# Optimization experiments

Measured on AMD Instinct MI355X. Metric: run time of the kernel, lower is better.

## Reference

```python
import jax, jax.numpy as jnp
from jax import lax
import numpy as np

UNITS = 128
IN_DIM = 512
BATCH = 128
SEQ = 1024


def setup_inputs() -> dict:
    key = jax.random.key(0)
    k1, k2, k3 = jax.random.split(key, 3)
    x = jax.random.normal(k1, (BATCH, SEQ, IN_DIM), dtype=jnp.float32)
    # glorot-ish scaling for stability
    W = jax.random.normal(k2, (IN_DIM, 4 * UNITS), dtype=jnp.float32) * (1.0 / np.sqrt(IN_DIM))
    U = jax.random.normal(k3, (UNITS, 4 * UNITS), dtype=jnp.float32) * (1.0 / np.sqrt(UNITS))
    b = jnp.zeros((4 * UNITS,), dtype=jnp.float32)
    return {"x": x, "W": W, "U": U, "b": b}


def reference(x, W, U, b):
    # Keras LSTM with activation='tanh' AND recurrent_activation='tanh'
    # (all four gates use tanh, unlike the standard sigmoid gates).
    # Gate order in Keras kernels: i, f, g(cell candidate), o.
    B = x.shape[0]
    units = U.shape[0]
    # Precompute input projections for all timesteps: [T, B, 4*units]
    xW = jnp.einsum('bti,ij->tbj', x, W) + b

    def step(carry, xw_t):
        h, c = carry
        z = xw_t + h @ U  # [B, 4*units]
        i, f, g, o = jnp.split(z, 4, axis=-1)
        i = jnp.tanh(i)
        f = jnp.tanh(f)
        g = jnp.tanh(g)
        o = jnp.tanh(o)
        c_new = f * c + i * g
        h_new = o * jnp.tanh(c_new)
        return (h_new, c_new), None

    h0 = jnp.zeros((B, units), dtype=x.dtype)
    c0 = jnp.zeros((B, units), dtype=x.dtype)
    (h_last, _), _ = lax.scan(step, (h0, c0), xW)
    return h_last  # [B, units] (return_sequences=False)
```

## Files before the change

kernel.cpp:

```cpp
#include <hip/hip_runtime.h>
#include <hip/hip_bf16.h>


#define UNITS 128
#define IN_DIM 512
#define BATCH 128
#define SEQ 1024
#define GATES 512
#define M_ROWS (BATCH * SEQ)

typedef __attribute__((ext_vector_type(8))) short short8;
typedef __attribute__((ext_vector_type(4))) float floatx4;
typedef __attribute__((ext_vector_type(4))) float fv4;
typedef __attribute__((ext_vector_type(2))) float fv2;

__device__ __forceinline__ unsigned short f2bf(float f) {
    unsigned int x = __builtin_bit_cast(unsigned int, f);
    unsigned int r = (x + 0x7fffu + ((x >> 16) & 1u)) >> 16;
    return (unsigned short)r;
}
__device__ __forceinline__ float bf2f(unsigned short u) {
    unsigned int x = ((unsigned int)u) << 16;
    return __builtin_bit_cast(float, x);
}
__device__ __forceinline__ unsigned int pack2(float lo, float hi) {
    return (unsigned int)f2bf(lo) | ((unsigned int)f2bf(hi) << 16);
}

__device__ __forceinline__ float fast_tanh(float x) {
    float y = fminf(34.6f, fmaxf(-34.6f, x * 2.88539008f));
    float e = __builtin_amdgcn_exp2f(y);
    return 1.0f - 2.0f * __builtin_amdgcn_rcpf(e + 1.0f);
}

template <int CTRL>
__device__ __forceinline__ float dppf(float x) {
    int xi = __builtin_bit_cast(int, x);
    int r = __builtin_amdgcn_update_dpp(0, xi, CTRL, 0xF, 0xF, true);
    return __builtin_bit_cast(float, r);
}
#define DPP_XOR1 0xB1
#define DPP_XOR2 0x4E
#define DPP_BC0 0x00
#define DPP_BC1 0x55
#define DPP_BC2 0xAA
#define DPP_BC3 0xFF

__device__ __forceinline__ void pk_fma(fv2& acc, fv2 a, fv2 b) {
    asm("v_pk_fma_f32 %0, %1, %2, %0" : "+v"(acc) : "v"(a), "v"(b));
}

__global__ void k_wt(const float* __restrict__ W, unsigned short* __restrict__ Wt) {
    int idx = blockIdx.x * 256 + threadIdx.x;
    int n = idx >> 9;
    int k = idx & 511;
    Wt[idx] = f2bf(W[k * 512 + n]);
}

template <bool XWF32>
__global__ void __launch_bounds__(256, 2)
k_gemm(const float* __restrict__ A, const unsigned short* __restrict__ Bt,
       void* __restrict__ Cout) {
    __shared__ __align__(16) unsigned short As[128 * 40];
    __shared__ __align__(16) unsigned short Bs[128 * 40];
    const int tid = threadIdx.x;
    const int m0 = blockIdx.y << 7;
    const int n0 = blockIdx.x << 7;
    const int l = tid & 63;
    const int w = tid >> 6;
    const int wr = (w >> 1) << 6;
    const int wc = (w & 1) << 6;
    const int lrow = l & 15;
    const int lq = l >> 4;

    floatx4 acc[4][4] = {};

    const int srow = tid >> 1;
    const int soff = (tid & 1) << 4;
    const float* ap = A + (size_t)(m0 + srow) * 512 + soff;
    const unsigned short* bp = Bt + (size_t)(n0 + srow) * 512 + soff;
    unsigned short* as = &As[srow * 40 + soff];
    unsigned short* bs = &Bs[srow * 40 + soff];

    for (int k0 = 0; k0 < 512; k0 += 32) {
        float4 a0 = *(const float4*)(ap + k0);
        float4 a1 = *(const float4*)(ap + k0 + 4);
        float4 a2 = *(const float4*)(ap + k0 + 8);
        float4 a3 = *(const float4*)(ap + k0 + 12);
        uint4 b0 = *(const uint4*)(bp + k0);
        uint4 b1 = *(const uint4*)(bp + k0 + 8);
        __syncthreads();
        uint4 pa0, pa1;
        pa0.x = pack2(a0.x, a0.y); pa0.y = pack2(a0.z, a0.w);
        pa0.z = pack2(a1.x, a1.y); pa0.w = pack2(a1.z, a1.w);
        pa1.x = pack2(a2.x, a2.y); pa1.y = pack2(a2.z, a2.w);
        pa1.z = pack2(a3.x, a3.y); pa1.w = pack2(a3.z, a3.w);
        *(uint4*)as = pa0;
        *(uint4*)(as + 8) = pa1;
        *(uint4*)bs = b0;
        *(uint4*)(bs + 8) = b1;
        __syncthreads();
        short8 af[4], bfv[4];
#pragma unroll
        for (int mi = 0; mi < 4; ++mi)
            af[mi] = *(const short8*)&As[(wr + mi * 16 + lrow) * 40 + lq * 8];
#pragma unroll
        for (int ni = 0; ni < 4; ++ni)
            bfv[ni] = *(const short8*)&Bs[(wc + ni * 16 + lrow) * 40 + lq * 8];
#pragma unroll
        for (int mi = 0; mi < 4; ++mi)
#pragma unroll
            for (int ni = 0; ni < 4; ++ni)
                acc[mi][ni] = __builtin_amdgcn_mfma_f32_16x16x32_bf16(
                    af[mi], bfv[ni], acc[mi][ni], 0, 0, 0);
    }
#pragma unroll
    for (int mi = 0; mi < 4; ++mi) {
#pragma unroll
        for (int ni = 0; ni < 4; ++ni) {
            int row = m0 + wr + mi * 16 + lq * 4;
            int col = n0 + wc + ni * 16 + lrow;
            if (XWF32) {
                float* Cf = (float*)Cout;
#pragma unroll
                for (int r = 0; r < 4; ++r)
                    Cf[(size_t)(row + r) * 512 + col] = acc[mi][ni][r];
            } else {
                unsigned short* Cb = (unsigned short*)Cout;
#pragma unroll
                for (int r = 0; r < 4; ++r)
                    Cb[(size_t)(row + r) * 512 + col] = f2bf(acc[mi][ni][r]);
            }
        }
    }
}

template <bool XWF32>
__global__ void __launch_bounds__(512, 1)
k_scan(const void* __restrict__ xwv, const float* __restrict__ U,
       const float* __restrict__ bias, float* __restrict__ out) {
    __shared__ __align__(16) float hbuf[2 * 160];
    const int j = threadIdx.x;
    const int bb = blockIdx.x;
    const int m = j >> 2;
    const int r = j & 3;

    fv2 u2[4][16];
#pragma unroll
    for (int i = 0; i < 16; ++i) {
        const float* Up0 = U + (size_t)(r * 32 + 2 * i) * 512 + m;
        const float* Up1 = Up0 + 512;
        u2[0][i] = (fv2){Up0[0], Up1[0]};
        u2[1][i] = (fv2){Up0[128], Up1[128]};
        u2[2][i] = (fv2){Up0[256], Up1[256]};
        u2[3][i] = (fv2){Up0[384], Up1[384]};
    }
    const float bj = bias[r * 128 + m];
    const int p = r & 1;
    const int q = (r >> 1) & 1;

    if (j < 160) hbuf[j] = 0.0f;
    __syncthreads();

    const float* xwf = (const float*)xwv + (size_t)bb * SEQ * 512 + r * 128 + m;
    const unsigned short* xwb =
        (const unsigned short*)xwv + (size_t)bb * SEQ * 512 + r * 128 + m;

    float c = 0.0f, hval = 0.0f;
    float xb_cur = (XWF32 ? xwf[0] : bf2f(xwb[0])) + bj;
    for (int t = 0; t < SEQ; ++t) {
        float xw_next = 0.0f;
        if (t + 1 < SEQ)
            xw_next = XWF32 ? xwf[(size_t)(t + 1) * 512]
                            : bf2f(xwb[(size_t)(t + 1) * 512]);

        fv2 A0 = {0.f, 0.f}, A1 = {0.f, 0.f}, A2 = {0.f, 0.f}, A3 = {0.f, 0.f};
        const fv4* h4 =
            (const fv4*)(hbuf + (t & 1) * 160 + r * 40);
#pragma unroll
        for (int i = 0; i < 8; ++i) {
            fv4 hv = h4[i];
            fv2 hl = hv.lo;
            fv2 hh = hv.hi;
            pk_fma(A0, hl, u2[0][2 * i]);
            pk_fma(A1, hl, u2[1][2 * i]);
            pk_fma(A2, hl, u2[2][2 * i]);
            pk_fma(A3, hl, u2[3][2 * i]);
            pk_fma(A0, hh, u2[0][2 * i + 1]);
            pk_fma(A1, hh, u2[1][2 * i + 1]);
            pk_fma(A2, hh, u2[2][2 * i + 1]);
            pk_fma(A3, hh, u2[3][2 * i + 1]);
        }
        float s0 = A0.x + A0.y;
        float s1 = A1.x + A1.y;
        float s2 = A2.x + A2.y;
        float s3 = A3.x + A3.y;

        float va = p ? s1 : s0;
        float oa = p ? s0 : s1;
        float vb = p ? s3 : s2;
        float ob = p ? s2 : s3;
        float a01 = va + dppf<DPP_XOR1>(oa);
        float a23 = vb + dppf<DPP_XOR1>(ob);
        float vv = q ? a23 : a01;
        float oo = q ? a01 : a23;
        float sigma = vv + dppf<DPP_XOR2>(oo);

        float tg = fast_tanh(sigma + xb_cur);

        float gi = dppf<DPP_BC0>(tg);
        float gf = dppf<DPP_BC1>(tg);
        float gg = dppf<DPP_BC2>(tg);
        float go = dppf<DPP_BC3>(tg);
        c = fmaf(gf, c, gi * gg);
        hval = go * fast_tanh(c);

        if (r == 0)
            hbuf[((t + 1) & 1) * 160 + (m >> 5) * 40 + (m & 31)] = hval;
        __syncthreads();
        xb_cur = xw_next + bj;
    }
    if (r == 0) out[bb * UNITS + m] = hval;
}

extern "C" void kernel_launch(void* const* d_in, const int* in_sizes, int n_in,
                              void* d_out, int out_size, void* d_ws, size_t ws_size,
                              hipStream_t stream) {
    const float* x = (const float*)d_in[0];
    const float* W = (const float*)d_in[1];
    const float* U = (const float*)d_in[2];
    const float* b = (const float*)d_in[3];
    float* out = (float*)d_out;

    char* ws = (char*)d_ws;
    const size_t WT_BYTES = (size_t)512 * 512 * 2;
    unsigned short* Wt = (unsigned short*)ws;
    void* xw = (void*)(ws + WT_BYTES);
    const size_t XW_F32_BYTES = (size_t)M_ROWS * 512 * 4;
    const bool f32path = (ws_size >= WT_BYTES + XW_F32_BYTES);

    k_wt<<<dim3(1024), dim3(256), 0, stream>>>(W, Wt);

    dim3 ggrid(4, 1024);
    if (f32path) {
        k_gemm<true><<<ggrid, dim3(256), 0, stream>>>(x, Wt, xw);
        k_scan<true><<<dim3(128), dim3(512), 0, stream>>>(xw, U, b, out);
    } else {
        k_gemm<false><<<ggrid, dim3(256), 0, stream>>>(x, Wt, xw);
        k_scan<false><<<dim3(128), dim3(512), 0, stream>>>(xw, U, b, out);
    }
}
```

Before: 1.043 ms.

## Halve scan block size, each thread computes two hidden units

```diff
diff --git a/kernel.cpp b/kernel.cpp
--- a/kernel.cpp
+++ b/kernel.cpp
@@ -136,45 +136,55 @@
 }
 
 template <bool XWF32>
-__global__ void __launch_bounds__(512, 1)
+__global__ void __launch_bounds__(256, 1)
 k_scan(const void* __restrict__ xwv, const float* __restrict__ U,
        const float* __restrict__ bias, float* __restrict__ out) {
     __shared__ __align__(16) float hbuf[2 * 160];
     const int j = threadIdx.x;
     const int bb = blockIdx.x;
-    const int m = j >> 2;
+    const int cp = j >> 2;
     const int r = j & 3;
 
-    fv2 u2[4][16];
+    fv2 u2[2][4][16];
 #pragma unroll
     for (int i = 0; i < 16; ++i) {
-        const float* Up0 = U + (size_t)(r * 32 + 2 * i) * 512 + m;
+        const float* Up0 = U + (size_t)(r * 32 + 2 * i) * 512;
         const float* Up1 = Up0 + 512;
-        u2[0][i] = (fv2){Up0[0], Up1[0]};
-        u2[1][i] = (fv2){Up0[128], Up1[128]};
-        u2[2][i] = (fv2){Up0[256], Up1[256]};
-        u2[3][i] = (fv2){Up0[384], Up1[384]};
-    }
-    const float bj = bias[r * 128 + m];
+#pragma unroll
+        for (int g = 0; g < 4; ++g) {
+            u2[0][g][i] = (fv2){Up0[g * 128 + cp], Up1[g * 128 + cp]};
+            u2[1][g][i] = (fv2){Up0[g * 128 + cp + 64], Up1[g * 128 + cp + 64]};
+        }
+    }
+    const float bA = bias[r * 128 + cp];
+    const float bB = bias[r * 128 + cp + 64];
     const int p = r & 1;
     const int q = (r >> 1) & 1;
 
     if (j < 160) hbuf[j] = 0.0f;
     __syncthreads();
 
-    const float* xwf = (const float*)xwv + (size_t)bb * SEQ * 512 + r * 128 + m;
-    const unsigned short* xwb =
-        (const unsigned short*)xwv + (size_t)bb * SEQ * 512 + r * 128 + m;
-
-    float c = 0.0f, hval = 0.0f;
-    float xb_cur = (XWF32 ? xwf[0] : bf2f(xwb[0])) + bj;
+    const float* xwfA = (const float*)xwv + (size_t)bb * SEQ * 512 + r * 128 + cp;
+    const unsigned short* xwbA =
+        (const unsigned short*)xwv + (size_t)bb * SEQ * 512 + r * 128 + cp;
+
+    float cA = 0.0f, cB = 0.0f, hA = 0.0f, hB = 0.0f;
+    float xbA = (XWF32 ? xwfA[0] : bf2f(xwbA[0])) + bA;
+    float xbB = (XWF32 ? xwfA[64] : bf2f(xwbA[64])) + bB;
     for (int t = 0; t < SEQ; ++t) {
-        float xw_next = 0.0f;
-        if (t + 1 < SEQ)
-            xw_next = XWF32 ? xwf[(size_t)(t + 1) * 512]
-                            : bf2f(xwb[(size_t)(t + 1) * 512]);
-
-        fv2 A0 = {0.f, 0.f}, A1 = {0.f, 0.f}, A2 = {0.f, 0.f}, A3 = {0.f, 0.f};
+        float xwA_n = 0.0f, xwB_n = 0.0f;
+        if (t + 1 < SEQ) {
+            if (XWF32) {
+                xwA_n = xwfA[(size_t)(t + 1) * 512];
+                xwB_n = xwfA[(size_t)(t + 1) * 512 + 64];
+            } else {
+                xwA_n = bf2f(xwbA[(size_t)(t + 1) * 512]);
+                xwB_n = bf2f(xwbA[(size_t)(t + 1) * 512 + 64]);
+            }
+        }
+
+        fv2 aA0 = {0.f, 0.f}, aA1 = {0.f, 0.f}, aA2 = {0.f, 0.f}, aA3 = {0.f, 0.f};
+        fv2 aB0 = {0.f, 0.f}, aB1 = {0.f, 0.f}, aB2 = {0.f, 0.f}, aB3 = {0.f, 0.f};
         const fv4* h4 =
             (const fv4*)(hbuf + (t & 1) * 160 + r * 40);
 #pragma unroll
@@ -182,45 +192,66 @@
             fv4 hv = h4[i];
             fv2 hl = hv.lo;
             fv2 hh = hv.hi;
-            pk_fma(A0, hl, u2[0][2 * i]);
-            pk_fma(A1, hl, u2[1][2 * i]);
-            pk_fma(A2, hl, u2[2][2 * i]);
-            pk_fma(A3, hl, u2[3][2 * i]);
-            pk_fma(A0, hh, u2[0][2 * i + 1]);
-            pk_fma(A1, hh, u2[1][2 * i + 1]);
-            pk_fma(A2, hh, u2[2][2 * i + 1]);
-            pk_fma(A3, hh, u2[3][2 * i + 1]);
-        }
-        float s0 = A0.x + A0.y;
-        float s1 = A1.x + A1.y;
-        float s2 = A2.x + A2.y;
-        float s3 = A3.x + A3.y;
-
-        float va = p ? s1 : s0;
-        float oa = p ? s0 : s1;
-        float vb = p ? s3 : s2;
-        float ob = p ? s2 : s3;
-        float a01 = va + dppf<DPP_XOR1>(oa);
-        float a23 = vb + dppf<DPP_XOR1>(ob);
-        float vv = q ? a23 : a01;
-        float oo = q ? a01 : a23;
-        float sigma = vv + dppf<DPP_XOR2>(oo);
-
-        float tg = fast_tanh(sigma + xb_cur);
-
-        float gi = dppf<DPP_BC0>(tg);
-        float gf = dppf<DPP_BC1>(tg);
-        float gg = dppf<DPP_BC2>(tg);
-        float go = dppf<DPP_BC3>(tg);
-        c = fmaf(gf, c, gi * gg);
-        hval = go * fast_tanh(c);
-
-        if (r == 0)
-            hbuf[((t + 1) & 1) * 160 + (m >> 5) * 40 + (m & 31)] = hval;
+            pk_fma(aA0, hl, u2[0][0][2 * i]);
+            pk_fma(aA1, hl, u2[0][1][2 * i]);
+            pk_fma(aA2, hl, u2[0][2][2 * i]);
+            pk_fma(aA3, hl, u2[0][3][2 * i]);
+            pk_fma(aB0, hl, u2[1][0][2 * i]);
+            pk_fma(aB1, hl, u2[1][1][2 * i]);
+            pk_fma(aB2, hl, u2[1][2][2 * i]);
+            pk_fma(aB3, hl, u2[1][3][2 * i]);
+            pk_fma(aA0, hh, u2[0][0][2 * i + 1]);
+            pk_fma(aA1, hh, u2[0][1][2 * i + 1]);
+            pk_fma(aA2, hh, u2[0][2][2 * i + 1]);
+            pk_fma(aA3, hh, u2[0][3][2 * i + 1]);
+            pk_fma(aB0, hh, u2[1][0][2 * i + 1]);
+            pk_fma(aB1, hh, u2[1][1][2 * i + 1]);
+            pk_fma(aB2, hh, u2[1][2][2 * i + 1]);
+            pk_fma(aB3, hh, u2[1][3][2 * i + 1]);
+        }
+        float sA0 = aA0.x + aA0.y, sA1 = aA1.x + aA1.y;
+        float sA2 = aA2.x + aA2.y, sA3 = aA3.x + aA3.y;
+        float sB0 = aB0.x + aB0.y, sB1 = aB1.x + aB1.y;
+        float sB2 = aB2.x + aB2.y, sB3 = aB3.x + aB3.y;
+
+        float vaA = p ? sA1 : sA0, oaA = p ? sA0 : sA1;
+        float vbA = p ? sA3 : sA2, obA = p ? sA2 : sA3;
+        float vaB = p ? sB1 : sB0, oaB = p ? sB0 : sB1;
+        float vbB = p ? sB3 : sB2, obB = p ? sB2 : sB3;
+        float a01A = vaA + dppf<DPP_XOR1>(oaA);
+        float a23A = vbA + dppf<DPP_XOR1>(obA);
+        float a01B = vaB + dppf<DPP_XOR1>(oaB);
+        float a23B = vbB + dppf<DPP_XOR1>(obB);
+        float vvA = q ? a23A : a01A, ooA = q ? a01A : a23A;
+        float vvB = q ? a23B : a01B, ooB = q ? a01B : a23B;
+        float sigA = vvA + dppf<DPP_XOR2>(ooA);
+        float sigB = vvB + dppf<DPP_XOR2>(ooB);
+
+        float tgA = fast_tanh(sigA + xbA);
+        float tgB = fast_tanh(sigB + xbB);
+
+        float giA = dppf<DPP_BC0>(tgA), gfA = dppf<DPP_BC1>(tgA);
+        float ggA = dppf<DPP_BC2>(tgA), goA = dppf<DPP_BC3>(tgA);
+        float giB = dppf<DPP_BC0>(tgB), gfB = dppf<DPP_BC1>(tgB);
+        float ggB = dppf<DPP_BC2>(tgB), goB = dppf<DPP_BC3>(tgB);
+        cA = fmaf(gfA, cA, giA * ggA);
+        cB = fmaf(gfB, cB, giB * ggB);
+        hA = goA * fast_tanh(cA);
+        hB = goB * fast_tanh(cB);
+
+        if (r == 0) {
+            float* nb = hbuf + ((t + 1) & 1) * 160;
+            nb[(cp >> 5) * 40 + (cp & 31)] = hA;
+            nb[((cp >> 5) + 2) * 40 + (cp & 31)] = hB;
+        }
         __syncthreads();
-        xb_cur = xw_next + bj;
-    }
-    if (r == 0) out[bb * UNITS + m] = hval;
+        xbA = xwA_n + bA;
+        xbB = xwB_n + bB;
+    }
+    if (r == 0) {
+        out[bb * UNITS + cp] = hA;
+        out[bb * UNITS + cp + 64] = hB;
+    }
 }
 
 extern "C" void kernel_launch(void* const* d_in, const int* in_sizes, int n_in,
@@ -244,9 +275,9 @@
     dim3 ggrid(4, 1024);
     if (f32path) {
         k_gemm<true><<<ggrid, dim3(256), 0, stream>>>(x, Wt, xw);
-        k_scan<true><<<dim3(128), dim3(512), 0, stream>>>(xw, U, b, out);
+        k_scan<true><<<dim3(128), dim3(256), 0, stream>>>(xw, U, b, out);
     } else {
         k_gemm<false><<<ggrid, dim3(256), 0, stream>>>(x, Wt, xw);
-        k_scan<false><<<dim3(128), dim3(512), 0, stream>>>(xw, U, b, out);
-    }
-}
+        k_scan<false><<<dim3(128), dim3(256), 0, stream>>>(xw, U, b, out);
+    }
+}
```

Result: slower. 1.351 ms (+29.5%).

## Split recurrent dot product across 8 lanes with two columns per thread group

Applied to the files above, without the earlier changes.

```diff
diff --git a/kernel.cpp b/kernel.cpp
--- a/kernel.cpp
+++ b/kernel.cpp
@@ -41,6 +41,7 @@
 }
 #define DPP_XOR1 0xB1
 #define DPP_XOR2 0x4E
+#define DPP_HMIR 0x141
 #define DPP_BC0 0x00
 #define DPP_BC1 0x55
 #define DPP_BC2 0xAA
@@ -142,85 +143,103 @@
     __shared__ __align__(16) float hbuf[2 * 160];
     const int j = threadIdx.x;
     const int bb = blockIdx.x;
-    const int m = j >> 2;
-    const int r = j & 3;
-
-    fv2 u2[4][16];
-#pragma unroll
-    for (int i = 0; i < 16; ++i) {
-        const float* Up0 = U + (size_t)(r * 32 + 2 * i) * 512 + m;
+    const int e = j & 7;
+    const int cg = j >> 3;
+
+    fv2 u2[8][8];
+#pragma unroll
+    for (int i = 0; i < 8; ++i) {
+        const float* Up0 = U + (size_t)(16 * e + 2 * i) * 512;
         const float* Up1 = Up0 + 512;
-        u2[0][i] = (fv2){Up0[0], Up1[0]};
-        u2[1][i] = (fv2){Up0[128], Up1[128]};
-        u2[2][i] = (fv2){Up0[256], Up1[256]};
-        u2[3][i] = (fv2){Up0[384], Up1[384]};
-    }
-    const float bj = bias[r * 128 + m];
-    const int p = r & 1;
-    const int q = (r >> 1) & 1;
-
-    if (j < 160) hbuf[j] = 0.0f;
+#pragma unroll
+        for (int g = 0; g < 4; ++g) {
+            u2[g][i] = (fv2){Up0[g * 128 + cg], Up1[g * 128 + cg]};
+            u2[4 + g][i] = (fv2){Up0[g * 128 + cg + 64], Up1[g * 128 + cg + 64]};
+        }
+    }
+    const int f1 = (e ^ (e >> 2)) & 1;
+    const int f2 = ((e >> 1) ^ (e >> 2)) & 1;
+    const int f3 = (e >> 2) & 1;
+    const int myg = f1 + 2 * f2;
+    const int mycol = cg + (f3 << 6);
+    const int gidx = myg * 128 + mycol;
+    const float bj = bias[gidx];
+
+    if (j < 320) hbuf[j] = 0.0f;
     __syncthreads();
 
-    const float* xwf = (const float*)xwv + (size_t)bb * SEQ * 512 + r * 128 + m;
+    const float* xwf = (const float*)xwv + (size_t)bb * SEQ * 512 + gidx;
     const unsigned short* xwb =
-        (const unsigned short*)xwv + (size_t)bb * SEQ * 512 + r * 128 + m;
+        (const unsigned short*)xwv + (size_t)bb * SEQ * 512 + gidx;
 
     float c = 0.0f, hval = 0.0f;
     float xb_cur = (XWF32 ? xwf[0] : bf2f(xwb[0])) + bj;
+    const int wslot = ((mycol >> 4) * 20) + (mycol & 15);
+
     for (int t = 0; t < SEQ; ++t) {
         float xw_next = 0.0f;
         if (t + 1 < SEQ)
             xw_next = XWF32 ? xwf[(size_t)(t + 1) * 512]
                             : bf2f(xwb[(size_t)(t + 1) * 512]);
 
-        fv2 A0 = {0.f, 0.f}, A1 = {0.f, 0.f}, A2 = {0.f, 0.f}, A3 = {0.f, 0.f};
-        const fv4* h4 =
-            (const fv4*)(hbuf + (t & 1) * 160 + r * 40);
-#pragma unroll
-        for (int i = 0; i < 8; ++i) {
+        fv2 a0 = {0.f, 0.f}, a1 = {0.f, 0.f}, a2 = {0.f, 0.f}, a3 = {0.f, 0.f};
+        fv2 a4 = {0.f, 0.f}, a5 = {0.f, 0.f}, a6 = {0.f, 0.f}, a7 = {0.f, 0.f};
+        const fv4* h4 = (const fv4*)(hbuf + (t & 1) * 160 + e * 20);
+#pragma unroll
+        for (int i = 0; i < 4; ++i) {
             fv4 hv = h4[i];
             fv2 hl = hv.lo;
             fv2 hh = hv.hi;
-            pk_fma(A0, hl, u2[0][2 * i]);
-            pk_fma(A1, hl, u2[1][2 * i]);
-            pk_fma(A2, hl, u2[2][2 * i]);
-            pk_fma(A3, hl, u2[3][2 * i]);
-            pk_fma(A0, hh, u2[0][2 * i + 1]);
-            pk_fma(A1, hh, u2[1][2 * i + 1]);
-            pk_fma(A2, hh, u2[2][2 * i + 1]);
-            pk_fma(A3, hh, u2[3][2 * i + 1]);
+            pk_fma(a0, hl, u2[0][2 * i]);
+            pk_fma(a1, hl, u2[1][2 * i]);
+            pk_fma(a2, hl, u2[2][2 * i]);
+            pk_fma(a3, hl, u2[3][2 * i]);
+            pk_fma(a4, hl, u2[4][2 * i]);
+            pk_fma(a5, hl, u2[5][2 * i]);
+            pk_fma(a6, hl, u2[6][2 * i]);
+            pk_fma(a7, hl, u2[7][2 * i]);
+            pk_fma(a0, hh, u2[0][2 * i + 1]);
+            pk_fma(a1, hh, u2[1][2 * i + 1]);
+            pk_fma(a2, hh, u2[2][2 * i + 1]);
+            pk_fma(a3, hh, u2[3][2 * i + 1]);
+            pk_fma(a4, hh, u2[4][2 * i + 1]);
+            pk_fma(a5, hh, u2[5][2 * i + 1]);
+            pk_fma(a6, hh, u2[6][2 * i + 1]);
+            pk_fma(a7, hh, u2[7][2 * i + 1]);
         }
-        float s0 = A0.x + A0.y;
-        float s1 = A1.x + A1.y;
-        float s2 = A2.x + A2.y;
-        float s3 = A3.x + A3.y;
-
-        float va = p ? s1 : s0;
-        float oa = p ? s0 : s1;
-        float vb = p ? s3 : s2;
-        float ob = p ? s2 : s3;
-        float a01 = va + dppf<DPP_XOR1>(oa);
-        float a23 = vb + dppf<DPP_XOR1>(ob);
-        float vv = q ? a23 : a01;
-        float oo = q ? a01 : a23;
-        float sigma = vv + dppf<DPP_XOR2>(oo);
-
-        float tg = fast_tanh(sigma + xb_cur);
-
-        float gi = dppf<DPP_BC0>(tg);
-        float gf = dppf<DPP_BC1>(tg);
-        float gg = dppf<DPP_BC2>(tg);
-        float go = dppf<DPP_BC3>(tg);
+        float s0 = a0.x + a0.y, s1 = a1.x + a1.y;
+        float s2 = a2.x + a2.y, s3 = a3.x + a3.y;
+        float s4 = a4.x + a4.y, s5 = a5.x + a5.y;
+        float s6 = a6.x + a6.y, s7 = a7.x + a7.y;
+
+        float t0 = (f1 ? s1 : s0) + dppf<DPP_XOR1>(f1 ? s0 : s1);
+        float t1 = (f1 ? s3 : s2) + dppf<DPP_XOR1>(f1 ? s2 : s3);
+        float t2 = (f1 ? s5 : s4) + dppf<DPP_XOR1>(f1 ? s4 : s5);
+        float t3 = (f1 ? s7 : s6) + dppf<DPP_XOR1>(f1 ? s6 : s7);
+        float v0 = (f2 ? t1 : t0) + dppf<DPP_XOR2>(f2 ? t0 : t1);
+        float v1 = (f2 ? t3 : t2) + dppf<DPP_XOR2>(f2 ? t2 : t3);
+        float sig = (f3 ? v1 : v0) + dppf<DPP_HMIR>(f3 ? v0 : v1);
+
+        float tg = fast_tanh(sig + xb_cur);
+
+        float q0 = dppf<DPP_BC0>(tg);
+        float q1 = dppf<DPP_BC1>(tg);
+        float q2 = dppf<DPP_BC2>(tg);
+        float q3 = dppf<DPP_BC3>(tg);
+        const bool hi = f3;
+        float gi = hi ? q3 : q0;
+        float gf = hi ? q2 : q1;
+        float gg = hi ? q1 : q2;
+        float go = hi ? q0 : q3;
         c = fmaf(gf, c, gi * gg);
         hval = go * fast_tanh(c);
 
-        if (r == 0)
-            hbuf[((t + 1) & 1) * 160 + (m >> 5) * 40 + (m & 31)] = hval;
+        if ((e & 3) == 0)
+            hbuf[((t + 1) & 1) * 160 + wslot] = hval;
         __syncthreads();
         xb_cur = xw_next + bj;
     }
-    if (r == 0) out[bb * UNITS + m] = hval;
+    if ((e & 3) == 0) out[bb * UNITS + mycol] = hval;
 }
 
 extern "C" void kernel_launch(void* const* d_in, const int* in_sizes, int n_in,
```

Measured after the change: 1.123 ms. +7.7%, slower.
